# Performance work log

Hardware: AMD Instinct MI355X
Metric: run time of the kernel (lower is better)

Reference implementation:

```python
import jax, jax.numpy as jnp
import numpy as np

B, T, V, H, L = 32, 128, 50257, 1024, 2


def setup_inputs() -> dict:
    key = jax.random.key(0)
    ks = jax.random.split(key, 8)
    s_in = 0.02   # small init to keep gates unsaturated
    return {
        "tokens": jax.random.randint(ks[0], (B, T), 0, V, dtype=jnp.int32),
        "embedding": jax.random.normal(ks[1], (V, H), jnp.float32) * s_in,
        "W_ih": jax.random.normal(ks[2], (L, 4 * H, H), jnp.float32) * s_in,
        "W_hh": jax.random.normal(ks[3], (L, 4 * H, H), jnp.float32) * s_in,
        "b_ih": jax.random.normal(ks[4], (L, 4 * H), jnp.float32) * s_in,
        "b_hh": jax.random.normal(ks[5], (L, 4 * H), jnp.float32) * s_in,
        "W_out": jax.random.normal(ks[6], (V, H), jnp.float32) * s_in,
        "b_out": jax.random.normal(ks[7], (V,), jnp.float32) * s_in,
        "h0": jnp.zeros((L, B, H), jnp.float32),
        "c0": jnp.zeros((L, B, H), jnp.float32),
    }


def reference(tokens, embedding, W_ih, W_hh, b_ih, b_hh, W_out, b_out, h0, c0):
    # Teacher-forced LSTM LM: embed -> L-layer LSTM (PyTorch gate order i,f,g,o)
    # -> vocab projection -> log-softmax. Dropout is identity (p=0 / eval).
    x = embedding[tokens]                      # [B,T,H]
    xs = jnp.swapaxes(x, 0, 1)                 # [T,B,H] time-major for scan
    n_layers = W_ih.shape[0]

    def step(carry, x_t):
        h, c = carry                           # each [L,B,H]
        inp = x_t
        hs, cs = [], []
        for l in range(n_layers):
            gates = inp @ W_ih[l].T + b_ih[l] + h[l] @ W_hh[l].T + b_hh[l]  # [B,4H]
            i_g, f_g, g_g, o_g = jnp.split(gates, 4, axis=-1)
            i_g = jax.nn.sigmoid(i_g)
            f_g = jax.nn.sigmoid(f_g)
            g_g = jnp.tanh(g_g)
            o_g = jax.nn.sigmoid(o_g)
            c_new = f_g * c[l] + i_g * g_g
            h_new = o_g * jnp.tanh(c_new)
            hs.append(h_new)
            cs.append(c_new)
            inp = h_new
        return (jnp.stack(hs), jnp.stack(cs)), inp

    (hT, cT), outs = jax.lax.scan(step, (h0, c0), xs)   # outs: [T,B,H]
    outs = jnp.swapaxes(outs, 0, 1)                     # [B,T,H]
    logits = outs @ W_out.T + b_out                     # [B,T,V]
    logp = jax.nn.log_softmax(logits, axis=-1)
    return logp, hT, cT
```

## Files before the change

kernel.cpp:

```cpp
#include <hip/hip_runtime.h>
#include <cstdint>
#include <cstddef>

#define DEVI __device__ __forceinline__

typedef __attribute__((ext_vector_type(8))) short short8;
typedef __attribute__((ext_vector_type(4))) float f32x4;
using u16 = unsigned short;

constexpr int BSZ = 32, TSZ = 128, VSZ = 50257, HSZ = 1024;
constexpr int M4 = BSZ * TSZ;
constexpr int FH = 4 * HSZ;
constexpr long long OUT_LOGP = (long long)M4 * VSZ;
constexpr int NWRK = 192;
constexpr int NBLK = 256;
constexpr int LDSB = 147584;
constexpr int LDBF = 50258;

DEVI u16 f2bf(float f) {
  unsigned u = __float_as_uint(f);
  unsigned r = (u + 0x7fffu + ((u >> 16) & 1u)) >> 16;
  return (u16)r;
}
DEVI float bf2f(u16 u) { return __uint_as_float(((unsigned)u) << 16); }
DEVI float sigm(float x) { return 1.f / (1.f + __expf(-x)); }
DEVI float tanh_fast(float x) { return 1.f - 2.f / (1.f + __expf(2.f * x)); }

DEVI f32x4 mfma16(short8 a, short8 b, f32x4 c) {
  return __builtin_amdgcn_mfma_f32_16x16x32_bf16(a, b, c, 0, 0, 0);
}

DEVI void gld16(const void* g, void* l) {
  auto gp = (const __attribute__((address_space(1))) unsigned int*)g;
  auto lp = (__attribute__((address_space(3))) unsigned int*)l;
  __builtin_amdgcn_global_load_lds(gp, lp, 16, 0, 0);
}

DEVI void cohld16x16(const u16* base, short8 (&d)[16]) {
  asm volatile(
      "global_load_dwordx4 %0, %16, off sc0 sc1\n\t"
      "global_load_dwordx4 %1, %16, off offset:64 sc0 sc1\n\t"
      "global_load_dwordx4 %2, %16, off offset:128 sc0 sc1\n\t"
      "global_load_dwordx4 %3, %16, off offset:192 sc0 sc1\n\t"
      "global_load_dwordx4 %4, %16, off offset:256 sc0 sc1\n\t"
      "global_load_dwordx4 %5, %16, off offset:320 sc0 sc1\n\t"
      "global_load_dwordx4 %6, %16, off offset:384 sc0 sc1\n\t"
      "global_load_dwordx4 %7, %16, off offset:448 sc0 sc1\n\t"
      "global_load_dwordx4 %8, %16, off offset:512 sc0 sc1\n\t"
      "global_load_dwordx4 %9, %16, off offset:576 sc0 sc1\n\t"
      "global_load_dwordx4 %10, %16, off offset:640 sc0 sc1\n\t"
      "global_load_dwordx4 %11, %16, off offset:704 sc0 sc1\n\t"
      "global_load_dwordx4 %12, %16, off offset:768 sc0 sc1\n\t"
      "global_load_dwordx4 %13, %16, off offset:832 sc0 sc1\n\t"
      "global_load_dwordx4 %14, %16, off offset:896 sc0 sc1\n\t"
      "global_load_dwordx4 %15, %16, off offset:960 sc0 sc1\n\t"
      "s_waitcnt vmcnt(0)"
      : "=&v"(d[0]), "=&v"(d[1]), "=&v"(d[2]), "=&v"(d[3]),
        "=&v"(d[4]), "=&v"(d[5]), "=&v"(d[6]), "=&v"(d[7]),
        "=&v"(d[8]), "=&v"(d[9]), "=&v"(d[10]), "=&v"(d[11]),
        "=&v"(d[12]), "=&v"(d[13]), "=&v"(d[14]), "=&v"(d[15])
      : "v"(base)
      : "memory");
}
DEVI void cohst2_u16(u16* p0, u16 v0, u16* p1, u16 v1) {
  asm volatile(
      "global_store_short %0, %2, off sc0 sc1\n\t"
      "global_store_short %1, %3, off sc0 sc1\n\t"
      "s_waitcnt vmcnt(0)"
      :: "v"(p0), "v"(p1), "v"((unsigned)v0), "v"((unsigned)v1)
      : "memory");
}
DEVI void cohst1_u16(u16* p0, u16 v0) {
  asm volatile(
      "global_store_short %0, %1, off sc0 sc1\n\t"
      "s_waitcnt vmcnt(0)"
      :: "v"(p0), "v"((unsigned)v0)
      : "memory");
}
DEVI void flagst(unsigned* p, unsigned v) {
  __hip_atomic_store(p, v, __ATOMIC_RELAXED, __HIP_MEMORY_SCOPE_AGENT);
}
DEVI unsigned flagld(const unsigned* p) {
  return __hip_atomic_load(p, __ATOMIC_RELAXED, __HIP_MEMORY_SCOPE_AGENT);
}

DEVI void wait64(const unsigned* f, unsigned g, int l) {
  while (!__all((int)(flagld(f + l) >= g))) __builtin_amdgcn_s_sleep(1);
}
DEVI void wait128(const unsigned* f, unsigned g, int l) {
  for (;;) {
    unsigned a = flagld(f + l);
    unsigned b = flagld(f + 64 + l);
    if (__all((int)((a >= g) && (b >= g)))) break;
    __builtin_amdgcn_s_sleep(1);
  }
}

__global__ void prep_misc(const float* __restrict__ bih, const float* __restrict__ bhh,
                          float* __restrict__ bias0, float* __restrict__ rowsum,
                          unsigned* __restrict__ bar) {
  int i = blockIdx.x * 256 + threadIdx.x;
  if (i < FH) { bias0[i] = bih[i] + bhh[i]; rowsum[i] = 0.f; }
  if (i < 1024) bar[i] = 0u;
}

__global__ void prep_h(const float* __restrict__ h0, u16* __restrict__ H0,
                       u16* __restrict__ h1init) {
  int i = blockIdx.x * 256 + threadIdx.x;
  H0[i] = f2bf(h0[i]);
  h1init[i] = f2bf(h0[BSZ * HSZ + i]);
}

__global__ void cvt_bf16(const float* __restrict__ src, u16* __restrict__ dst, int n4) {
  int i = blockIdx.x * blockDim.x + threadIdx.x;
  int stride = gridDim.x * blockDim.x;
  for (; i < n4; i += stride) {
    float4 v = ((const float4*)src)[i];
    ushort4 o; o.x = f2bf(v.x); o.y = f2bf(v.y); o.z = f2bf(v.z); o.w = f2bf(v.w);
    ((ushort4*)dst)[i] = o;
  }
}

__global__ __launch_bounds__(256) void embed_kernel(const int* __restrict__ tok,
                                                    const float* __restrict__ emb,
                                                    u16* __restrict__ X) {
  int m = blockIdx.x;
  int t = m >> 5, b = m & 31;
  int token = tok[b * TSZ + t];
  const float4* src = (const float4*)(emb + (size_t)token * HSZ);
  int i = threadIdx.x;
  float4 v = src[i];
  ushort4 o; o.x = f2bf(v.x); o.y = f2bf(v.y); o.z = f2bf(v.z); o.w = f2bf(v.w);
  *(ushort4*)(X + (size_t)m * HSZ + i * 4) = o;
}

template <int EPI, bool BCVT, int MAP>
__global__ __launch_bounds__(256) void gemm_bt(const u16* __restrict__ A,
                                               const void* __restrict__ Bsrc,
                                               void* __restrict__ Cout,
                                               const float* __restrict__ bias,
                                               float* __restrict__ rowsum,
                                               int nm, int nn, int N, int K, int ldc) {
  __shared__ char smemg[16384];
  u16* As = (u16*)smemg;
  u16* Bs = (u16*)(smemg + 8192);
  float* epi = (float*)smemg;
  const int tid = threadIdx.x;
  int gsz = nm * nn;
  int id = blockIdx.x;
  int bm, bn;
  if constexpr (MAP == 1) {
    const int xcd = id & 7, idx = id >> 3;
    bn = idx >> 2;
    bm = (xcd << 2) + (idx & 3);
  } else {
    int wg = ((gsz & 7) == 0) ? (id % 8) * (gsz >> 3) + (id >> 3) : id;
    bm = wg % nm; bn = wg / nm;
  }
  const int m0 = bm * 128, n0 = bn * 128;
  const int l = tid & 63, wid = tid >> 6;
  const int wm = wid >> 1, wn = wid & 1;

  const int srow = tid >> 2, sq = tid & 3;
  const int arow0 = m0 + srow, arow1 = m0 + 64 + srow;
  int brow0 = n0 + srow;      if (brow0 > N - 1) brow0 = N - 1;
  int brow1 = n0 + 64 + srow; if (brow1 > N - 1) brow1 = N - 1;

  const u16* Bbf = (const u16*)Bsrc;
  const float* Bf32 = (const float*)Bsrc;
  u16* AsW = As + (size_t)(tid >> 6) * 512;
  u16* BsW = Bs + (size_t)(tid >> 6) * 512;

  f32x4 acc[4][4];
  f32x4 z = {0.f, 0.f, 0.f, 0.f};
#pragma unroll
  for (int a = 0; a < 4; ++a)
#pragma unroll
    for (int b = 0; b < 4; ++b) acc[a][b] = z;

  for (int k0 = 0; k0 < K; k0 += 32) {
    gld16(A + (size_t)arow0 * K + k0 + sq * 8, AsW);
    gld16(A + (size_t)arow1 * K + k0 + sq * 8, AsW + 2048);
    if (!BCVT) {
      gld16(Bbf + (size_t)brow0 * K + k0 + sq * 8, BsW);
      gld16(Bbf + (size_t)brow1 * K + k0 + sq * 8, BsW + 2048);
    } else {
      const float* s0 = Bf32 + (size_t)brow0 * K + k0 + sq * 8;
      const float* s1 = Bf32 + (size_t)brow1 * K + k0 + sq * 8;
      float4 x0 = *(const float4*)s0, y0 = *(const float4*)(s0 + 4);
      float4 x1 = *(const float4*)s1, y1 = *(const float4*)(s1 + 4);
      short8 v0, v1;
      v0[0]=(short)f2bf(x0.x); v0[1]=(short)f2bf(x0.y); v0[2]=(short)f2bf(x0.z); v0[3]=(short)f2bf(x0.w);
      v0[4]=(short)f2bf(y0.x); v0[5]=(short)f2bf(y0.y); v0[6]=(short)f2bf(y0.z); v0[7]=(short)f2bf(y0.w);
      v1[0]=(short)f2bf(x1.x); v1[1]=(short)f2bf(x1.y); v1[2]=(short)f2bf(x1.z); v1[3]=(short)f2bf(x1.w);
      v1[4]=(short)f2bf(y1.x); v1[5]=(short)f2bf(y1.y); v1[6]=(short)f2bf(y1.z); v1[7]=(short)f2bf(y1.w);
      *(short8*)&Bs[(size_t)tid * 8] = v0;
      *(short8*)&Bs[(size_t)tid * 8 + 2048] = v1;
    }
    __syncthreads();
    short8 af[4], bfr[4];
#pragma unroll
    for (int x = 0; x < 4; ++x) {
      int ar = wm * 64 + x * 16 + (l & 15);
      af[x] = *(const short8*)&As[ar * 32 + ((l >> 4) << 3)];
      int br = wn * 64 + x * 16 + (l & 15);
      bfr[x] = *(const short8*)&Bs[br * 32 + ((l >> 4) << 3)];
    }
#pragma unroll
    for (int mf = 0; mf < 4; ++mf)
#pragma unroll
      for (int nf = 0; nf < 4; ++nf)
        acc[mf][nf] = mfma16(af[mf], bfr[nf], acc[mf][nf]);
    __syncthreads();
  }

  if constexpr (EPI == 2) {
    u16* C = (u16*)Cout;
#pragma unroll
    for (int mf = 0; mf < 4; ++mf) {
      int rbase = m0 + wm * 64 + mf * 16 + ((l >> 4) << 2);
      float bvr[4];
#pragma unroll
      for (int j = 0; j < 4; ++j) bvr[j] = bias[rbase + j];
#pragma unroll
      for (int nf = 0; nf < 4; ++nf) {
        int cg = n0 + wn * 64 + nf * 16 + (l & 15);
#pragma unroll
        for (int j = 0; j < 4; ++j)
          C[(size_t)(rbase + j) * ldc + cg] = f2bf(acc[mf][nf][j] + bvr[j]);
      }
    }
  } else if constexpr (EPI == 3) {
    u16* C = (u16*)Cout;
    float* ep = epi + wid * 1024;
    const int lq4 = l >> 4, l15e = l & 15;
    float bv[4];
#pragma unroll
    for (int nf = 0; nf < 4; ++nf) {
      int cg = n0 + wn * 64 + nf * 16 + l15e;
      bv[nf] = (cg < N) ? bias[cg] : 0.f;
    }
    const int r8 = l >> 3, c8 = l & 7;
    const int colb8 = n0 + wn * 64 + c8 * 8;
#pragma unroll
    for (int mf = 0; mf < 4; ++mf) {
#pragma unroll
      for (int nf = 0; nf < 4; ++nf)
#pragma unroll
        for (int j = 0; j < 4; ++j)
          ep[(lq4 * 4 + j) * 64 + nf * 16 + l15e] = acc[mf][nf][j] + bv[nf];
      asm volatile("s_waitcnt lgkmcnt(0)" ::: "memory");
      __builtin_amdgcn_sched_barrier(0);
#pragma unroll
      for (int pass = 0; pass < 2; ++pass) {
        const int rr = pass * 8 + r8;
        f32x4 v0 = *(const f32x4*)&ep[rr * 64 + c8 * 8];
        f32x4 v1 = *(const f32x4*)&ep[rr * 64 + c8 * 8 + 4];
        const int row = m0 + wm * 64 + mf * 16 + rr;
        float e = 0.f;
        if (colb8 + 7 < N) {
          short8 o;
          o[0]=(short)f2bf(v0[0]); o[1]=(short)f2bf(v0[1]);
          o[2]=(short)f2bf(v0[2]); o[3]=(short)f2bf(v0[3]);
          o[4]=(short)f2bf(v1[0]); o[5]=(short)f2bf(v1[1]);
          o[6]=(short)f2bf(v1[2]); o[7]=(short)f2bf(v1[3]);
          *(short8*)&C[(size_t)row * ldc + colb8] = o;
          e = __expf(v0[0]) + __expf(v0[1]) + __expf(v0[2]) + __expf(v0[3]) +
              __expf(v1[0]) + __expf(v1[1]) + __expf(v1[2]) + __expf(v1[3]);
        } else {
#pragma unroll
          for (int kk = 0; kk < 8; ++kk) {
            float fv = (kk < 4) ? v0[kk] : v1[kk - 4];
            if (colb8 + kk < N) {
              C[(size_t)row * ldc + colb8 + kk] = f2bf(fv);
              e += __expf(fv);
            }
          }
        }
        e += __shfl_xor(e, 1, 8); e += __shfl_xor(e, 2, 8); e += __shfl_xor(e, 4, 8);
        if (c8 == 0) atomicAdd(&rowsum[row], e);
      }
      asm volatile("s_waitcnt lgkmcnt(0)" ::: "memory");
      __builtin_amdgcn_sched_barrier(0);
    }
  } else {
    float* C = (float*)Cout;
    float* ep = epi + wid * 1024;
    const int lq4 = l >> 4, l15e = l & 15;
    float bv[4];
#pragma unroll
    for (int nf = 0; nf < 4; ++nf) {
      int cg = n0 + wn * 64 + nf * 16 + l15e;
      bv[nf] = (cg < N) ? bias[cg] : 0.f;
    }
    const int colbase = n0 + wn * 64 + l15e * 4;
#pragma unroll
    for (int mf = 0; mf < 4; ++mf) {
#pragma unroll
      for (int nf = 0; nf < 4; ++nf)
#pragma unroll
        for (int j = 0; j < 4; ++j)
          ep[(lq4 * 4 + j) * 64 + nf * 16 + l15e] = acc[mf][nf][j] + bv[nf];
      asm volatile("s_waitcnt lgkmcnt(0)" ::: "memory");
      __builtin_amdgcn_sched_barrier(0);
#pragma unroll
      for (int pass = 0; pass < 4; ++pass) {
        const int rr = pass * 4 + lq4;
        f32x4 v = *(const f32x4*)&ep[rr * 64 + l15e * 4];
        const int row = m0 + wm * 64 + mf * 16 + rr;
        float e = 0.f;
        if (colbase + 3 < N) {
          *(f32x4*)&C[(size_t)row * ldc + colbase] = v;
          e = __expf(v[0]) + __expf(v[1]) + __expf(v[2]) + __expf(v[3]);
        } else {
#pragma unroll
          for (int kk = 0; kk < 4; ++kk)
            if (colbase + kk < N) {
              C[(size_t)row * ldc + colbase + kk] = v[kk];
              e += __expf(v[kk]);
            }
        }
        e += __shfl_xor(e, 1, 16); e += __shfl_xor(e, 2, 16);
        e += __shfl_xor(e, 4, 16); e += __shfl_xor(e, 8, 16);
        if (l15e == 0) atomicAdd(&rowsum[row], e);
      }
      asm volatile("s_waitcnt lgkmcnt(0)" ::: "memory");
      __builtin_amdgcn_sched_barrier(0);
    }
  }
}

struct LstmArgs {
  const u16* G0T;
  const float* Wih;
  const float* Whh;
  const float* bih, *bhh, *c0;
  u16* H0;
  u16* H1;
  const u16* h1init;
  float* out_hc;
  unsigned* bar;
  const float* Wout;
  u16* Woutbf;
  int docvt;
};

DEVI void stage_row_q(const float* src, char* row, int sw, int q) {
  for (int kk = 0; kk < 256; kk += 8) {
    float4 x = *(const float4*)(src + kk);
    float4 y = *(const float4*)(src + kk + 4);
    short8 v;
    v[0]=(short)f2bf(x.x); v[1]=(short)f2bf(x.y); v[2]=(short)f2bf(x.z); v[3]=(short)f2bf(x.w);
    v[4]=(short)f2bf(y.x); v[5]=(short)f2bf(y.y); v[6]=(short)f2bf(y.z); v[7]=(short)f2bf(y.w);
    const int kbyte = (q * 256 + kk) * 2;
    *(short8*)(row + (kbyte ^ sw)) = v;
  }
}

DEVI short8 ldsB(const char* lds, int r, int kbyte) {
  return *(const short8*)(lds + (size_t)r * 2048 + (kbyte ^ ((r & 7) << 4)));
}

DEVI void part_wr(float* part, int wstride_log2, int wv, int R, int lq, f32x4 v) {
  *(f32x4*)&part[(wv << wstride_log2) + (R << 4) + ((lq ^ (R & 3)) << 2)] = v;
}
DEVI float part_rd(const float* part, int wstride_log2, int wv, int R, int c) {
  return part[(wv << wstride_log2) + (R << 4) + ((((c >> 2) ^ (R & 3)) << 2)) + (c & 3)];
}

__global__ __launch_bounds__(256, 1) void lstm_coop(LstmArgs A) {
  extern __shared__ char smem[];
  const int wg = blockIdx.x, tid = threadIdx.x;
  const int wv = tid >> 6, l = tid & 63;
  const int l15 = l & 15, lq = l >> 4;
  const int bh = wv >> 1, kh = wv & 1;

  if (wg < 64) {
    char* WL = smem;
    float* part = (float*)(smem + 131072);
    const int j0 = wg << 4;
    {
      const int R = tid >> 2, q = tid & 3;
      const int grow = ((R >> 4) << 10) + j0 + (R & 15);
      stage_row_q(A.Whh + (size_t)grow * HSZ + q * 256, WL + (size_t)R * 2048,
                  (R & 7) << 4, q);
    }
    const int uu = tid & 15, bb = tid >> 4;
    float cst[2];
    cst[0] = A.c0[(size_t)bb * HSZ + j0 + uu];
    cst[1] = A.c0[(size_t)(bb + 16) * HSZ + j0 + uu];
    __syncthreads();
    unsigned* myflag = A.bar + wg;

    for (int t = 0; t < TSZ; ++t) {
      float g0v[4][2];
      {
        const int col = t * 32;
#pragma unroll
        for (int g4 = 0; g4 < 4; ++g4) {
          const u16* gp = A.G0T + (size_t)((g4 << 10) + j0 + uu) * M4 + col;
          g0v[g4][0] = bf2f(gp[bb]);
          g0v[g4][1] = bf2f(gp[bb + 16]);
        }
      }
      if (t > 0) wait64(A.bar, (unsigned)t, l);
      const u16* hprev = A.H0 + (size_t)t * (BSZ * HSZ);
      const u16* hb = hprev + (size_t)(bh * 16 + l15) * HSZ + (kh << 9) + (lq << 3);
      short8 a[16];
      cohld16x16(hb, a);
      __builtin_amdgcn_sched_barrier(0);
      f32x4 acc[4];
      { f32x4 z = {0.f,0.f,0.f,0.f}; acc[0]=z; acc[1]=z; acc[2]=z; acc[3]=z; }
#pragma unroll
      for (int k = 0; k < 16; ++k) {
        const int kbyte = (((kh << 4) + k) << 6) + (lq << 4);
#pragma unroll
        for (int tr = 0; tr < 4; ++tr)
          acc[tr] = mfma16(a[k], ldsB(WL, (tr << 4) + l15, kbyte), acc[tr]);
      }
#pragma unroll
      for (int tr = 0; tr < 4; ++tr)
        part_wr(part, 10, wv, (tr << 4) + l15, lq, acc[tr]);
      __syncthreads();
      const bool last = (t == TSZ - 1);
      u16* hnext = A.H0 + (size_t)(t + 1) * (BSZ * HSZ);
      u16 hv[2];
#pragma unroll
      for (int pp = 0; pp < 2; ++pp) {
        const int b = bb + (pp << 4);
        float gi = g0v[0][pp], gf = g0v[1][pp], gg = g0v[2][pp], go = g0v[3][pp];
#pragma unroll
        for (int kh2 = 0; kh2 < 2; ++kh2) {
          const int w2 = (pp << 1) | kh2;
          gi += part_rd(part, 10, w2, uu, bb);
          gf += part_rd(part, 10, w2, 16 + uu, bb);
          gg += part_rd(part, 10, w2, 32 + uu, bb);
          go += part_rd(part, 10, w2, 48 + uu, bb);
        }
        float i_ = sigm(gi), f_ = sigm(gf), g_ = tanh_fast(gg), o_ = sigm(go);
        float c_ = f_ * cst[pp] + i_ * g_;
        cst[pp] = c_;
        float h_ = o_ * tanh_fast(c_);
        hv[pp] = f2bf(h_);
        if (last) {
          A.out_hc[(size_t)b * HSZ + j0 + uu] = h_;
          A.out_hc[2 * BSZ * HSZ + (size_t)b * HSZ + j0 + uu] = c_;
        }
      }
      cohst2_u16(hnext + (size_t)bb * HSZ + j0 + uu, hv[0],
                 hnext + (size_t)(bb + 16) * HSZ + j0 + uu, hv[1]);
      __syncthreads();
      if (tid == 0) flagst(myflag, (unsigned)(t + 1));
    }
  } else if (wg < NWRK) {
    char* WxL = smem;
    char* WhL = smem + 65536;
    float* part = (float*)(smem + 131072);
    float* biasL = (float*)(smem + 139264);
    const int lw = wg - 64;
    const int j1 = lw << 3;
    {
      const int rr = tid >> 2, q = tid & 3;
      const int r = rr & 31;
      const int grow = FH + ((r >> 3) << 10) + j1 + (r & 7);
      const float* base = (rr >= 32) ? A.Whh : A.Wih;
      char* dst = ((rr >= 32) ? WhL : WxL) + (size_t)r * 2048;
      stage_row_q(base + (size_t)grow * HSZ + q * 256, dst, (r & 7) << 4, q);
    }
    if (tid < 32) {
      const int grow = FH + ((tid >> 3) << 10) + j1 + (tid & 7);
      biasL[tid] = A.bih[grow] + A.bhh[grow];
    }
    const int uu = tid & 7, b1 = tid >> 3;
    float cst = A.c0[BSZ * HSZ + (size_t)b1 * HSZ + j1 + uu];
    __syncthreads();
    unsigned* myflag = A.bar + 64 + lw;

    for (int t = 0; t < TSZ; ++t) {
      wait64(A.bar, (unsigned)(t + 1), l);
      const u16* x1 = A.H0 + (size_t)(t + 1) * (BSZ * HSZ);
      const u16* xb = x1 + (size_t)(bh * 16 + l15) * HSZ + (kh << 9) + (lq << 3);
      short8 ax[16];
      cohld16x16(xb, ax);
      __builtin_amdgcn_sched_barrier(0);
      f32x4 acc[2];
      { f32x4 z = {0.f,0.f,0.f,0.f}; acc[0]=z; acc[1]=z; }
#pragma unroll
      for (int k = 0; k < 16; ++k) {
        const int kbyte = (((kh << 4) + k) << 6) + (lq << 4);
        acc[0] = mfma16(ax[k], ldsB(WxL, l15, kbyte), acc[0]);
        acc[1] = mfma16(ax[k], ldsB(WxL, 16 + l15, kbyte), acc[1]);
      }
      if (t > 0) wait128(A.bar + 64, (unsigned)t, l);
      const u16* hp = (t == 0) ? A.h1init : A.H1 + (size_t)(t - 1) * HSZ;
      const size_t hstr = (t == 0) ? (size_t)HSZ : (size_t)TSZ * HSZ;
      const u16* hbp = hp + (size_t)(bh * 16 + l15) * hstr + (kh << 9) + (lq << 3);
      short8 ah[16];
      cohld16x16(hbp, ah);
      __builtin_amdgcn_sched_barrier(0);
#pragma unroll
      for (int k = 0; k < 16; ++k) {
        const int kbyte = (((kh << 4) + k) << 6) + (lq << 4);
        acc[0] = mfma16(ah[k], ldsB(WhL, l15, kbyte), acc[0]);
        acc[1] = mfma16(ah[k], ldsB(WhL, 16 + l15, kbyte), acc[1]);
      }
#pragma unroll
      for (int tr = 0; tr < 2; ++tr)
        part_wr(part, 9, wv, (tr << 4) + l15, lq, acc[tr]);
      __syncthreads();
      const bool last = (t == TSZ - 1);
      {
        const int c = b1 & 15, ph = b1 >> 4;
        float gi = biasL[uu], gf = biasL[8 + uu], gg = biasL[16 + uu], go = biasL[24 + uu];
#pragma unroll
        for (int kh2 = 0; kh2 < 2; ++kh2) {
          const int w2 = (ph << 1) | kh2;
          gi += part_rd(part, 9, w2, uu, c);
          gf += part_rd(part, 9, w2, 8 + uu, c);
          gg += part_rd(part, 9, w2, 16 + uu, c);
          go += part_rd(part, 9, w2, 24 + uu, c);
        }
        float i_ = sigm(gi), f_ = sigm(gf), g_ = tanh_fast(gg), o_ = sigm(go);
        float c_ = f_ * cst + i_ * g_;
        cst = c_;
        float h_ = o_ * tanh_fast(c_);
        cohst1_u16(A.H1 + (size_t)b1 * (TSZ * HSZ) + (size_t)t * HSZ + j1 + uu, f2bf(h_));
        if (last) {
          A.out_hc[BSZ * HSZ + (size_t)b1 * HSZ + j1 + uu] = h_;
          A.out_hc[3 * BSZ * HSZ + (size_t)b1 * HSZ + j1 + uu] = c_;
        }
      }
      __syncthreads();
      if (tid == 0) flagst(myflag, (unsigned)(t + 1));
    }
  } else {
    if (A.docvt) {
      const int n4 = (int)((size_t)VSZ * HSZ / 4);
      int i = (wg - NWRK) * 256 + tid;
      const int stride = 64 * 256;
      const float4* src = (const float4*)A.Wout;
      ushort4* dst = (ushort4*)A.Woutbf;
      for (; i < n4; i += stride) {
        float4 v = src[i];
        ushort4 o; o.x = f2bf(v.x); o.y = f2bf(v.y); o.z = f2bf(v.z); o.w = f2bf(v.w);
        dst[i] = o;
      }
    }
  }
}

__global__ void lse_kernel(float* __restrict__ rowsum, int n) {
  int i = blockIdx.x * 256 + threadIdx.x;
  if (i < n) rowsum[i] = logf(rowsum[i]);
}

__global__ __launch_bounds__(256) void lsm_finish(float* __restrict__ C,
                                                  const float* __restrict__ lse, int Vd) {
  int row = blockIdx.y;
  size_t start = (size_t)row * (size_t)Vd;
  float s = lse[row];
  int i = blockIdx.x * 256 + threadIdx.x;
  int col = i * 4;
  if (col + 3 < Vd) {
    f32x4* p = (f32x4*)(C + start + col);
    f32x4 v = *p;
    v[0] -= s; v[1] -= s; v[2] -= s; v[3] -= s;
    *p = v;
  } else {
    for (int j = col; j < Vd; ++j) C[start + j] -= s;
  }
}

__global__ __launch_bounds__(256) void lsm_finish_bf(const u16* __restrict__ L,
                                                     float* __restrict__ out,
                                                     const float* __restrict__ rowsum,
                                                     int Vd, int ldl) {
  int row = blockIdx.y;
  float s = logf(rowsum[row]);
  int col = blockIdx.x * 2048 + threadIdx.x * 8;
  const u16* lp = L + (size_t)row * ldl;
  float* op = out + (size_t)row * Vd;
  if (col + 7 < Vd) {
    short8 v = *(const short8*)(lp + col);
    f32x4 a, b;
    a[0] = bf2f((u16)v[0]) - s; a[1] = bf2f((u16)v[1]) - s;
    a[2] = bf2f((u16)v[2]) - s; a[3] = bf2f((u16)v[3]) - s;
    b[0] = bf2f((u16)v[4]) - s; b[1] = bf2f((u16)v[5]) - s;
    b[2] = bf2f((u16)v[6]) - s; b[3] = bf2f((u16)v[7]) - s;
    *(f32x4*)(op + col) = a;
    *(f32x4*)(op + col + 4) = b;
  } else {
    for (int j = col; j < Vd; ++j) op[j] = bf2f(lp[j]) - s;
  }
}

extern "C" void kernel_launch(void* const* d_in, const int* in_sizes, int n_in,
                              void* d_out, int out_size, void* d_ws, size_t ws_size,
                              hipStream_t stream) {
  const int* tokens = (const int*)d_in[0];
  const float* emb = (const float*)d_in[1];
  const float* Wih = (const float*)d_in[2];
  const float* Whh = (const float*)d_in[3];
  const float* bih = (const float*)d_in[4];
  const float* bhh = (const float*)d_in[5];
  const float* Wout = (const float*)d_in[6];
  const float* bout = (const float*)d_in[7];
  const float* h0 = (const float*)d_in[8];
  const float* c0 = (const float*)d_in[9];
  float* out = (float*)d_out;

  char* w = (char*)d_ws;
  size_t o = 0;
  u16* Xbf = (u16*)(w + o);    o += (size_t)M4 * HSZ * 2;
  u16* Wih0bf = (u16*)(w + o); o += (size_t)FH * HSZ * 2;
  u16* G0T = (u16*)(w + o);    o += (size_t)FH * M4 * 2;
  u16* H0 = (u16*)(w + o);     o += (size_t)(TSZ + 1) * BSZ * HSZ * 2;
  u16* H1 = (u16*)(w + o);     o += (size_t)BSZ * TSZ * HSZ * 2;
  u16* h1init = (u16*)(w + o); o += (size_t)BSZ * HSZ * 2;
  float* bias0 = (float*)(w + o);  o += FH * 4;
  float* rowsum = (float*)(w + o); o += M4 * 4;
  unsigned* bar = (unsigned*)(w + o); o += 4096;
  u16* Woutbf = (u16*)(w + o);
  size_t need_full = o + (size_t)VSZ * HSZ * 2;
  u16* Lbf = (u16*)(w + need_full);
  size_t need_lbf = need_full + (size_t)M4 * LDBF * 2;
  const bool bcvt = (ws_size < need_full);
  const bool bf16c = (ws_size >= need_lbf);

  prep_misc<<<16, 256, 0, stream>>>(bih, bhh, bias0, rowsum, bar);
  prep_h<<<128, 256, 0, stream>>>(h0, H0, h1init);
  cvt_bf16<<<2048, 256, 0, stream>>>(Wih, Wih0bf, FH * HSZ / 4);
  embed_kernel<<<M4, 256, 0, stream>>>(tokens, emb, Xbf);
  gemm_bt<2, false, 0><<<32 * 32, 256, 0, stream>>>(Wih0bf, Xbf, G0T, bias0, nullptr,
                                                    32, 32, M4, HSZ, M4);

  LstmArgs la{G0T, Wih, Whh, bih, bhh, c0, H0, H1, h1init,
              out + (size_t)OUT_LOGP, bar, Wout, Woutbf, bcvt ? 0 : 1};
  void* kargs[] = {&la};
  hipFuncSetAttribute((const void*)lstm_coop, hipFuncAttributeMaxDynamicSharedMemorySize, LDSB);
  hipLaunchCooperativeKernel((const void*)lstm_coop, dim3(NBLK), dim3(256), kargs, LDSB, stream);

  const int nn = (VSZ + 127) / 128;
  if (bf16c) {
    gemm_bt<3, false, 1><<<32 * nn, 256, 0, stream>>>(H1, Woutbf, Lbf, bout, rowsum,
                                                      32, nn, VSZ, HSZ, LDBF);
    lsm_finish_bf<<<dim3(25, M4), 256, 0, stream>>>(Lbf, out, rowsum, VSZ, LDBF);
  } else if (!bcvt) {
    gemm_bt<1, false, 1><<<32 * nn, 256, 0, stream>>>(H1, Woutbf, out, bout, rowsum,
                                                      32, nn, VSZ, HSZ, VSZ);
    lse_kernel<<<16, 256, 0, stream>>>(rowsum, M4);
    lsm_finish<<<dim3((VSZ + 1023) / 1024, M4), 256, 0, stream>>>(out, rowsum, VSZ);
  } else {
    gemm_bt<1, true, 1><<<32 * nn, 256, 0, stream>>>(H1, Wout, out, bout, rowsum,
                                                     32, nn, VSZ, HSZ, VSZ);
    lse_kernel<<<16, 256, 0, stream>>>(rowsum, M4);
    lsm_finish<<<dim3((VSZ + 1023) / 1024, M4), 256, 0, stream>>>(out, rowsum, VSZ);
  }
}
```

Before: 1.749 ms.

## Overlap vocab projection tiles with LSTM recurrence in idle cooperative blocks

```diff
diff --git a/kernel.cpp b/kernel.cpp
--- a/kernel.cpp
+++ b/kernel.cpp
@@ -1,4 +1,5 @@
 #include <hip/hip_runtime.h>
+#include <hip/hip_bf16.h>
 #include <cstdint>
 #include <cstddef>
 
@@ -16,11 +17,18 @@
 constexpr int NBLK = 256;
 constexpr int LDSB = 147584;
 constexpr int LDBF = 50258;
+constexpr int NNT = 393;
+constexpr int CVT_PER = 20;
+constexpr int CVTILES = 64 * CVT_PER;
 
 DEVI u16 f2bf(float f) {
   unsigned u = __float_as_uint(f);
   unsigned r = (u + 0x7fffu + ((u >> 16) & 1u)) >> 16;
   return (u16)r;
+}
+DEVI u16 f2bf_hw(float f) {
+  __hip_bfloat16 h = __float2bfloat16(f);
+  return __builtin_bit_cast(u16, h);
 }
 DEVI float bf2f(u16 u) { return __uint_as_float(((unsigned)u) << 16); }
 DEVI float sigm(float x) { return 1.f / (1.f + __expf(-x)); }
@@ -96,19 +104,15 @@
   }
 }
 
-__global__ void prep_misc(const float* __restrict__ bih, const float* __restrict__ bhh,
-                          float* __restrict__ bias0, float* __restrict__ rowsum,
-                          unsigned* __restrict__ bar) {
-  int i = blockIdx.x * 256 + threadIdx.x;
-  if (i < FH) { bias0[i] = bih[i] + bhh[i]; rowsum[i] = 0.f; }
-  if (i < 1024) bar[i] = 0u;
-}
-
-__global__ void prep_h(const float* __restrict__ h0, u16* __restrict__ H0,
-                       u16* __restrict__ h1init) {
+__global__ void prep_all(const float* __restrict__ bih, const float* __restrict__ bhh,
+                         float* __restrict__ bias0, float* __restrict__ rowsum,
+                         unsigned* __restrict__ bar, const float* __restrict__ h0,
+                         u16* __restrict__ H0, u16* __restrict__ h1init) {
   int i = blockIdx.x * 256 + threadIdx.x;
   H0[i] = f2bf(h0[i]);
   h1init[i] = f2bf(h0[BSZ * HSZ + i]);
+  if (i < FH) { bias0[i] = bih[i] + bhh[i]; rowsum[i] = 0.f; }
+  if (i < 1024) bar[i] = 0u;
 }
 
 __global__ void cvt_bf16(const float* __restrict__ src, u16* __restrict__ dst, int n4) {
@@ -134,30 +138,14 @@
   *(ushort4*)(X + (size_t)m * HSZ + i * 4) = o;
 }
 
-template <int EPI, bool BCVT, int MAP>
-__global__ __launch_bounds__(256) void gemm_bt(const u16* __restrict__ A,
-                                               const void* __restrict__ Bsrc,
-                                               void* __restrict__ Cout,
-                                               const float* __restrict__ bias,
-                                               float* __restrict__ rowsum,
-                                               int nm, int nn, int N, int K, int ldc) {
-  __shared__ char smemg[16384];
+template <int EPI, bool BCVT, bool TMAJ>
+DEVI void gemm_tile(char* smemg, const u16* __restrict__ A, const void* __restrict__ Bsrc,
+                    void* __restrict__ Cout, const float* __restrict__ bias,
+                    float* __restrict__ rowsum, int m0, int n0, int N, int K, int ldc) {
   u16* As = (u16*)smemg;
   u16* Bs = (u16*)(smemg + 8192);
   float* epi = (float*)smemg;
   const int tid = threadIdx.x;
-  int gsz = nm * nn;
-  int id = blockIdx.x;
-  int bm, bn;
-  if constexpr (MAP == 1) {
-    const int xcd = id & 7, idx = id >> 3;
-    bn = idx >> 2;
-    bm = (xcd << 2) + (idx & 3);
-  } else {
-    int wg = ((gsz & 7) == 0) ? (id % 8) * (gsz >> 3) + (id >> 3) : id;
-    bm = wg % nm; bn = wg / nm;
-  }
-  const int m0 = bm * 128, n0 = bn * 128;
   const int l = tid & 63, wid = tid >> 6;
   const int wm = wid >> 1, wn = wid & 1;
 
@@ -227,7 +215,7 @@
         int cg = n0 + wn * 64 + nf * 16 + (l & 15);
 #pragma unroll
         for (int j = 0; j < 4; ++j)
-          C[(size_t)(rbase + j) * ldc + cg] = f2bf(acc[mf][nf][j] + bvr[j]);
+          C[(size_t)(rbase + j) * ldc + cg] = f2bf_hw(acc[mf][nf][j] + bvr[j]);
       }
     }
   } else if constexpr (EPI == 3) {
@@ -257,14 +245,15 @@
         f32x4 v0 = *(const f32x4*)&ep[rr * 64 + c8 * 8];
         f32x4 v1 = *(const f32x4*)&ep[rr * 64 + c8 * 8 + 4];
         const int row = m0 + wm * 64 + mf * 16 + rr;
+        const int orow = TMAJ ? ((row & 31) * TSZ + (row >> 5)) : row;
         float e = 0.f;
         if (colb8 + 7 < N) {
           short8 o;
-          o[0]=(short)f2bf(v0[0]); o[1]=(short)f2bf(v0[1]);
-          o[2]=(short)f2bf(v0[2]); o[3]=(short)f2bf(v0[3]);
-          o[4]=(short)f2bf(v1[0]); o[5]=(short)f2bf(v1[1]);
-          o[6]=(short)f2bf(v1[2]); o[7]=(short)f2bf(v1[3]);
-          *(short8*)&C[(size_t)row * ldc + colb8] = o;
+          o[0]=(short)f2bf_hw(v0[0]); o[1]=(short)f2bf_hw(v0[1]);
+          o[2]=(short)f2bf_hw(v0[2]); o[3]=(short)f2bf_hw(v0[3]);
+          o[4]=(short)f2bf_hw(v1[0]); o[5]=(short)f2bf_hw(v1[1]);
+          o[6]=(short)f2bf_hw(v1[2]); o[7]=(short)f2bf_hw(v1[3]);
+          *(short8*)&C[(size_t)orow * ldc + colb8] = o;
           e = __expf(v0[0]) + __expf(v0[1]) + __expf(v0[2]) + __expf(v0[3]) +
               __expf(v1[0]) + __expf(v1[1]) + __expf(v1[2]) + __expf(v1[3]);
         } else {
@@ -272,13 +261,13 @@
           for (int kk = 0; kk < 8; ++kk) {
             float fv = (kk < 4) ? v0[kk] : v1[kk - 4];
             if (colb8 + kk < N) {
-              C[(size_t)row * ldc + colb8 + kk] = f2bf(fv);
+              C[(size_t)orow * ldc + colb8 + kk] = f2bf_hw(fv);
               e += __expf(fv);
             }
           }
         }
         e += __shfl_xor(e, 1, 8); e += __shfl_xor(e, 2, 8); e += __shfl_xor(e, 4, 8);
-        if (c8 == 0) atomicAdd(&rowsum[row], e);
+        if (c8 == 0) atomicAdd(&rowsum[orow], e);
       }
       asm volatile("s_waitcnt lgkmcnt(0)" ::: "memory");
       __builtin_amdgcn_sched_barrier(0);
@@ -308,26 +297,52 @@
         const int rr = pass * 4 + lq4;
         f32x4 v = *(const f32x4*)&ep[rr * 64 + l15e * 4];
         const int row = m0 + wm * 64 + mf * 16 + rr;
+        const int orow = TMAJ ? ((row & 31) * TSZ + (row >> 5)) : row;
         float e = 0.f;
         if (colbase + 3 < N) {
-          *(f32x4*)&C[(size_t)row * ldc + colbase] = v;
+          *(f32x4*)&C[(size_t)orow * ldc + colbase] = v;
           e = __expf(v[0]) + __expf(v[1]) + __expf(v[2]) + __expf(v[3]);
         } else {
 #pragma unroll
           for (int kk = 0; kk < 4; ++kk)
             if (colbase + kk < N) {
-              C[(size_t)row * ldc + colbase + kk] = v[kk];
+              C[(size_t)orow * ldc + colbase + kk] = v[kk];
               e += __expf(v[kk]);
             }
         }
         e += __shfl_xor(e, 1, 16); e += __shfl_xor(e, 2, 16);
         e += __shfl_xor(e, 4, 16); e += __shfl_xor(e, 8, 16);
-        if (l15e == 0) atomicAdd(&rowsum[row], e);
+        if (l15e == 0) atomicAdd(&rowsum[orow], e);
       }
       asm volatile("s_waitcnt lgkmcnt(0)" ::: "memory");
       __builtin_amdgcn_sched_barrier(0);
     }
   }
+}
+
+template <int EPI, bool BCVT, int MAP, bool TMAJ>
+__global__ __launch_bounds__(256) void gemm_bt(const u16* __restrict__ A,
+                                               const void* __restrict__ Bsrc,
+                                               void* __restrict__ Cout,
+                                               const float* __restrict__ bias,
+                                               float* __restrict__ rowsum,
+                                               int nm, int nn, int N, int K, int ldc,
+                                               int wofs) {
+  __shared__ char smemg[16384];
+  const int id = blockIdx.x;
+  int bm, bn;
+  if constexpr (MAP == 2) {
+    const int gsz = (int)gridDim.x;
+    int wg = ((gsz & 7) == 0) ? (id % 8) * (gsz >> 3) + (id >> 3) : id;
+    int w = wofs + wg;
+    bm = w / nn; bn = w % nn;
+  } else {
+    const int gsz = nm * nn;
+    int wg = ((gsz & 7) == 0) ? (id % 8) * (gsz >> 3) + (id >> 3) : id;
+    bm = wg % nm; bn = wg / nm;
+  }
+  gemm_tile<EPI, BCVT, TMAJ>(smemg, A, Bsrc, Cout, bias, rowsum,
+                             bm * 128, bn * 128, N, K, ldc);
 }
 
 struct LstmArgs {
@@ -342,7 +357,10 @@
   unsigned* bar;
   const float* Wout;
   u16* Woutbf;
-  int docvt;
+  u16* Lbf;
+  const float* bout;
+  float* rowsum;
+  int mode;
 };
 
 DEVI void stage_row_q(const float* src, char* row, int sw, int q) {
@@ -492,9 +510,8 @@
         acc[1] = mfma16(ax[k], ldsB(WxL, 16 + l15, kbyte), acc[1]);
       }
       if (t > 0) wait128(A.bar + 64, (unsigned)t, l);
-      const u16* hp = (t == 0) ? A.h1init : A.H1 + (size_t)(t - 1) * HSZ;
-      const size_t hstr = (t == 0) ? (size_t)HSZ : (size_t)TSZ * HSZ;
-      const u16* hbp = hp + (size_t)(bh * 16 + l15) * hstr + (kh << 9) + (lq << 3);
+      const u16* hp = (t == 0) ? A.h1init : A.H1 + (size_t)(t - 1) * (BSZ * HSZ);
+      const u16* hbp = hp + (size_t)(bh * 16 + l15) * HSZ + (kh << 9) + (lq << 3);
       short8 ah[16];
       cohld16x16(hbp, ah);
       __builtin_amdgcn_sched_barrier(0);
@@ -524,7 +541,7 @@
         float c_ = f_ * cst + i_ * g_;
         cst = c_;
         float h_ = o_ * tanh_fast(c_);
-        cohst1_u16(A.H1 + (size_t)b1 * (TSZ * HSZ) + (size_t)t * HSZ + j1 + uu, f2bf(h_));
+        cohst1_u16(A.H1 + (size_t)t * (BSZ * HSZ) + (size_t)b1 * HSZ + j1 + uu, f2bf(h_));
         if (last) {
           A.out_hc[BSZ * HSZ + (size_t)b1 * HSZ + j1 + uu] = h_;
           A.out_hc[3 * BSZ * HSZ + (size_t)b1 * HSZ + j1 + uu] = c_;
@@ -534,16 +551,32 @@
       if (tid == 0) flagst(myflag, (unsigned)(t + 1));
     }
   } else {
-    if (A.docvt) {
+    const int cid = wg - NWRK;
+    if (A.mode >= 1) {
       const int n4 = (int)((size_t)VSZ * HSZ / 4);
-      int i = (wg - NWRK) * 256 + tid;
-      const int stride = 64 * 256;
       const float4* src = (const float4*)A.Wout;
       ushort4* dst = (ushort4*)A.Woutbf;
-      for (; i < n4; i += stride) {
+      for (int i = cid * 256 + tid; i < n4; i += 64 * 256) {
         float4 v = src[i];
-        ushort4 o; o.x = f2bf(v.x); o.y = f2bf(v.y); o.z = f2bf(v.z); o.w = f2bf(v.w);
+        ushort4 o;
+        o.x = f2bf_hw(v.x); o.y = f2bf_hw(v.y); o.z = f2bf_hw(v.z); o.w = f2bf_hw(v.w);
         dst[i] = o;
+      }
+      asm volatile("s_waitcnt vmcnt(0)" ::: "memory");
+      __builtin_amdgcn_fence(__ATOMIC_RELEASE, "agent");
+      __syncthreads();
+      if (tid == 0) flagst(A.bar + 192 + cid, 1u);
+      if (A.mode == 2) {
+        wait64(A.bar + 192, 1u, l);
+        __syncthreads();
+        for (int k = 0; k < CVT_PER; ++k) {
+          const int w = cid + (k << 6);
+          const int bm = w / NNT, bn = w % NNT;
+          wait128(A.bar + 64, (unsigned)(4 * bm + 4), l);
+          __syncthreads();
+          gemm_tile<3, false, true>(smem, A.H1, A.Woutbf, A.Lbf, A.bout, A.rowsum,
+                                    bm * 128, bn * 128, VSZ, HSZ, LDBF);
+        }
       }
     }
   }
@@ -626,33 +659,33 @@
   size_t need_lbf = need_full + (size_t)M4 * LDBF * 2;
   const bool bcvt = (ws_size < need_full);
   const bool bf16c = (ws_size >= need_lbf);
-
-  prep_misc<<<16, 256, 0, stream>>>(bih, bhh, bias0, rowsum, bar);
-  prep_h<<<128, 256, 0, stream>>>(h0, H0, h1init);
+  const int mode = bcvt ? 0 : (bf16c ? 2 : 1);
+
+  prep_all<<<128, 256, 0, stream>>>(bih, bhh, bias0, rowsum, bar, h0, H0, h1init);
   cvt_bf16<<<2048, 256, 0, stream>>>(Wih, Wih0bf, FH * HSZ / 4);
   embed_kernel<<<M4, 256, 0, stream>>>(tokens, emb, Xbf);
-  gemm_bt<2, false, 0><<<32 * 32, 256, 0, stream>>>(Wih0bf, Xbf, G0T, bias0, nullptr,
-                                                    32, 32, M4, HSZ, M4);
+  gemm_bt<2, false, 0, false><<<32 * 32, 256, 0, stream>>>(
+      Wih0bf, Xbf, G0T, bias0, nullptr, 32, 32, M4, HSZ, M4, 0);
 
   LstmArgs la{G0T, Wih, Whh, bih, bhh, c0, H0, H1, h1init,
-              out + (size_t)OUT_LOGP, bar, Wout, Woutbf, bcvt ? 0 : 1};
+              out + (size_t)OUT_LOGP, bar, Wout, Woutbf, Lbf, bout, rowsum, mode};
   void* kargs[] = {&la};
   hipFuncSetAttribute((const void*)lstm_coop, hipFuncAttributeMaxDynamicSharedMemorySize, LDSB);
   hipLaunchCooperativeKernel((const void*)lstm_coop, dim3(NBLK), dim3(256), kargs, LDSB, stream);
 
-  const int nn = (VSZ + 127) / 128;
+  const int TOT = 32 * NNT;
   if (bf16c) {
-    gemm_bt<3, false, 1><<<32 * nn, 256, 0, stream>>>(H1, Woutbf, Lbf, bout, rowsum,
-                                                      32, nn, VSZ, HSZ, LDBF);
+    gemm_bt<3, false, 2, true><<<TOT - CVTILES, 256, 0, stream>>>(
+        H1, Woutbf, Lbf, bout, rowsum, 32, NNT, VSZ, HSZ, LDBF, CVTILES);
     lsm_finish_bf<<<dim3(25, M4), 256, 0, stream>>>(Lbf, out, rowsum, VSZ, LDBF);
   } else if (!bcvt) {
-    gemm_bt<1, false, 1><<<32 * nn, 256, 0, stream>>>(H1, Woutbf, out, bout, rowsum,
-                                                      32, nn, VSZ, HSZ, VSZ);
+    gemm_bt<1, false, 2, true><<<TOT, 256, 0, stream>>>(
+        H1, Woutbf, out, bout, rowsum, 32, NNT, VSZ, HSZ, VSZ, 0);
     lse_kernel<<<16, 256, 0, stream>>>(rowsum, M4);
     lsm_finish<<<dim3((VSZ + 1023) / 1024, M4), 256, 0, stream>>>(out, rowsum, VSZ);
   } else {
-    gemm_bt<1, true, 1><<<32 * nn, 256, 0, stream>>>(H1, Wout, out, bout, rowsum,
-                                                     32, nn, VSZ, HSZ, VSZ);
+    gemm_bt<1, true, 2, true><<<TOT, 256, 0, stream>>>(
+        H1, Wout, out, bout, rowsum, 32, NNT, VSZ, HSZ, VSZ, 0);
     lse_kernel<<<16, 256, 0, stream>>>(rowsum, M4);
     lsm_finish<<<dim3((VSZ + 1023) / 1024, M4), 256, 0, stream>>>(out, rowsum, VSZ);
   }
```

Result: no change. 1.764 ms (+0.9%).
